# Kernel tuning notes

Hardware: AMD Instinct MI355X
Metric: run time of the kernel (lower is better)

Reference implementation:

```python
import jax, jax.numpy as jnp
import numpy as np

NG, NT, E = 2500, 20000, 640000
SRC_DIM, DST_DIM, HID, OUT, NCLS = 128, 500, 128, 128, 16


def setup_inputs() -> dict:
    key = jax.random.key(0)
    ks = jax.random.split(key, 11)
    d = {
        "gene_feats": jax.random.normal(ks[0], (NG, SRC_DIM), jnp.float32),
        "train_feats": jax.random.normal(ks[1], (NT, DST_DIM), jnp.float32),
        "edge_src": jax.random.randint(ks[2], (E,), 0, NG),
        "edge_dst": jax.random.randint(ks[3], (E,), 0, NT),
        # conv1: SAGEConv((src_dim, dst_dim) -> hidden)
        "W1_neigh": jax.random.normal(ks[4], (SRC_DIM, HID), jnp.float32) / np.sqrt(SRC_DIM),
        "W1_self": jax.random.normal(ks[5], (DST_DIM, HID), jnp.float32) / np.sqrt(DST_DIM),
        "b1": jnp.zeros((HID,), jnp.float32),
        # conv2: SAGEConv(hidden -> out); src input is the raw gene features
        "W2_neigh": jax.random.normal(ks[6], (HID, OUT), jnp.float32) / np.sqrt(HID),
        "W2_self": jax.random.normal(ks[7], (HID, OUT), jnp.float32) / np.sqrt(HID),
        "b2": jnp.zeros((OUT,), jnp.float32),
        # classifier MLP
        "Wc1": jax.random.normal(ks[8], (OUT, OUT), jnp.float32) / np.sqrt(OUT),
        "bc1": jnp.zeros((OUT,), jnp.float32),
        "Wc2": jax.random.normal(ks[9], (OUT, NCLS), jnp.float32) / np.sqrt(OUT),
        "bc2": jnp.zeros((NCLS,), jnp.float32),
    }
    return d


def _segment_mean(msgs, dst, num_segments):
    # mean over in-edges; isolated dst nodes get 0 (DGL convention)
    sums = jax.ops.segment_sum(msgs, dst, num_segments=num_segments)
    cnt = jax.ops.segment_sum(jnp.ones((msgs.shape[0],), msgs.dtype), dst,
                              num_segments=num_segments)
    return sums / jnp.maximum(cnt, 1.0)[:, None]


def reference(gene_feats, train_feats, edge_src, edge_dst,
              W1_neigh, W1_self, b1, W2_neigh, W2_self, b2,
              Wc1, bc1, Wc2, bc2):
    # mean-aggregate gene (src) features onto train (dst) nodes
    agg = _segment_mean(gene_feats[edge_src], edge_dst, NT)  # [NT, SRC_DIM]
    # conv1: fc_self(h_dst) + fc_neigh(mean_neigh) + bias, then ReLU
    h1 = jax.nn.relu(train_feats @ W1_self + agg @ W1_neigh + b1)  # [NT, HID]
    # conv2 reuses raw gene features as src -> same mean aggregation
    h2 = jax.nn.relu(h1 @ W2_self + agg @ W2_neigh + b2)  # [NT, OUT]
    # classifier: Linear -> ReLU -> Linear
    return jax.nn.relu(h2 @ Wc1 + bc1) @ Wc2 + bc2  # [NT, NCLS]
```

## Files before the change

### kernel.cpp

```cpp
#include <hip/hip_runtime.h>


#define NG 2500
#define NT 20000
#define NE 640000
#define NCLS 16
#define CAP 96
#define BCAP 1536
#define NBIN 625

typedef unsigned short u16;
typedef unsigned int u32;

typedef float f32x4 __attribute__((ext_vector_type(4)));
typedef __bf16 bf16x8 __attribute__((ext_vector_type(8)));

__device__ __forceinline__ float b2f(u16 u) { return __uint_as_float(((u32)u) << 16); }
__device__ __forceinline__ float blo(u32 p) { return __uint_as_float(p << 16); }
__device__ __forceinline__ float bhi(u32 p) { return __uint_as_float(p & 0xffff0000u); }
__device__ __forceinline__ u16 f2b(float f) {
    u32 u = __float_as_uint(f);
    return (u16)((u + 0x7fffu + ((u >> 16) & 1u)) >> 16);
}

#define B1N 81920
#define B2N 32768
#define B3N 16384
#define B4N 2048
#define NEB 625
#define GNB 625
#define PKB 520

__global__ __launch_bounds__(256) void k_prep(
    const int* __restrict__ edst,
    u32* __restrict__ hist,
    const float* __restrict__ gene, u32* __restrict__ GH32,
    const float* __restrict__ W1n, const float* __restrict__ W1s,
    const float* __restrict__ W2n, const float* __restrict__ W2s,
    const float* __restrict__ Wc1, const float* __restrict__ Wc2,
    u16* __restrict__ B1h, u16* __restrict__ B1l,
    u16* __restrict__ B2h, u16* __restrict__ B2l,
    u16* __restrict__ B3h, u16* __restrict__ B3l,
    u16* __restrict__ B4h, u16* __restrict__ B4l) {
    int blk = blockIdx.x, t = threadIdx.x;
    if (blk < NEB) {
        __shared__ u32 lh[NBIN];
        for (int i = t; i < NBIN; i += 256) lh[i] = 0;
        __syncthreads();
        int e0 = (blk * 256 + t) * 4;
        const int4 d4 = *(const int4*)(edst + e0);
        int dd[4] = {d4.x, d4.y, d4.z, d4.w};
#pragma unroll
        for (int i = 0; i < 4; ++i) {
            unsigned d = (unsigned)dd[i];
            if (d < NT) atomicAdd(&lh[d >> 5], 1u);
        }
        __syncthreads();
        for (int i = t; i < NBIN; i += 256)
            hist[(size_t)blk * NBIN + i] = lh[i];
        return;
    }
    if (blk < NEB + GNB) {
        int idx = (blk - NEB) * 256 + t;
        float2 v = ((const float2*)gene)[idx];
        GH32[idx] = (u32)f2b(v.x) | ((u32)f2b(v.y) << 16);
        return;
    }
    int idx = (blk - NEB - GNB) * 256 + t;
    float v = 0.f;
    u16 *ph = 0, *pl = 0;
    int off = 0;
    if (idx < B1N) {
        int j = idx & 7, l = (idx >> 3) & 63, rest = idx >> 9;
        int g = rest & 7, kk = rest >> 3;
        int k = kk * 32 + ((l >> 4) << 3) + j, n = (g << 4) + (l & 15);
        if (k < 500) v = W1s[k * 128 + n];
        else if (k >= 512) v = W1n[(k - 512) * 128 + n];
        ph = B1h; pl = B1l; off = idx;
    } else if (idx < B1N + B2N) {
        int e = idx - B1N;
        int j = e & 7, l = (e >> 3) & 63, rest = e >> 9;
        int g = rest & 7, kk = rest >> 3;
        int k = kk * 32 + ((l >> 4) << 3) + j, n = (g << 4) + (l & 15);
        v = (k < 128) ? W2s[k * 128 + n] : W2n[(k - 128) * 128 + n];
        ph = B2h; pl = B2l; off = e;
    } else if (idx < B1N + B2N + B3N) {
        int e = idx - (B1N + B2N);
        int j = e & 7, l = (e >> 3) & 63, rest = e >> 9;
        int g = rest & 7, kk = rest >> 3;
        int k = kk * 32 + ((l >> 4) << 3) + j, n = (g << 4) + (l & 15);
        v = Wc1[k * 128 + n];
        ph = B3h; pl = B3l; off = e;
    } else if (idx < B1N + B2N + B3N + B4N) {
        int e = idx - (B1N + B2N + B3N);
        int j = e & 7, l = (e >> 3) & 63, kk = e >> 9;
        int k = kk * 32 + ((l >> 4) << 3) + j, n = l & 15;
        v = Wc2[k * 16 + n];
        ph = B4h; pl = B4l; off = e;
    }
    if (ph) {
        u16 hi = f2b(v);
        u16 lo = f2b(v - b2f(hi));
        ph[off] = hi;
        pl[off] = lo;
    }
}

__global__ __launch_bounds__(256) void k_scan(
    const u32* __restrict__ hist, u32* __restrict__ boff,
    int* __restrict__ bcnt) {
    int bin = blockIdx.x, t = threadIdx.x;
    __shared__ u32 part[256];
    u32 s0 = 0, s1 = 0, s2 = 0;
    int i0 = 3 * t;
    if (i0 < NBIN) s0 = hist[(size_t)i0 * NBIN + bin];
    if (i0 + 1 < NBIN) s1 = hist[(size_t)(i0 + 1) * NBIN + bin];
    if (i0 + 2 < NBIN) s2 = hist[(size_t)(i0 + 2) * NBIN + bin];
    u32 mine = s0 + s1 + s2;
    part[t] = mine;
    __syncthreads();
    for (int off = 1; off < 256; off <<= 1) {
        u32 x = (t >= off) ? part[t - off] : 0u;
        __syncthreads();
        part[t] += x;
        __syncthreads();
    }
    u32 base = part[t] - mine;
    if (i0 < NBIN) boff[(size_t)bin * NBIN + i0] = base;
    if (i0 + 1 < NBIN) boff[(size_t)bin * NBIN + i0 + 1] = base + s0;
    if (i0 + 2 < NBIN) boff[(size_t)bin * NBIN + i0 + 2] = base + s0 + s1;
    if (t == 255) bcnt[bin] = (int)part[255];
}

__global__ __launch_bounds__(256) void k_scat(
    const int* __restrict__ esrc, const int* __restrict__ edst,
    const u32* __restrict__ boff, u32* __restrict__ bkt) {
    int blk = blockIdx.x, t = threadIdx.x;
    __shared__ u32 lcur[NBIN];
    for (int i = t; i < NBIN; i += 256) lcur[i] = 0;
    __syncthreads();
    int e0 = (blk * 256 + t) * 4;
    const int4 s4 = *(const int4*)(esrc + e0);
    const int4 d4 = *(const int4*)(edst + e0);
    int ss[4] = {s4.x, s4.y, s4.z, s4.w};
    int dd[4] = {d4.x, d4.y, d4.z, d4.w};
#pragma unroll
    for (int i = 0; i < 4; ++i) {
        unsigned d = (unsigned)dd[i];
        if (d < NT) {
            int bin = (int)(d >> 5);
            u32 rank = atomicAdd(&lcur[bin], 1u);
            u32 pos = boff[(size_t)bin * NBIN + blk] + rank;
            if (pos < BCAP)
                bkt[(size_t)bin * BCAP + pos] = ((d & 31u) << 16) | (u32)ss[i];
        }
    }
}

__global__ __launch_bounds__(512, 3) void k_mega(
    const int* __restrict__ bcnt, const u32* __restrict__ bkt,
    const u16* __restrict__ GH, const float* __restrict__ train,
    const u16* __restrict__ B1h, const u16* __restrict__ B1l,
    const u16* __restrict__ B2h, const u16* __restrict__ B2l,
    const u16* __restrict__ B3h, const u16* __restrict__ B3l,
    const u16* __restrict__ B4h, const u16* __restrict__ B4l,
    const float* __restrict__ b1, const float* __restrict__ b2,
    const float* __restrict__ bc1, const float* __restrict__ bc2,
    float* __restrict__ out) {
    __shared__ __align__(16) u16 SMEM[26112];
    __shared__ __align__(16) u16 SRT[32 * CAP];
    __shared__ int POS[32];
    u16* SAGh = SMEM;
    u16* SAGl = SMEM + 4352;
    u16* S1h = SMEM + 8704;
    u16* S1l = SMEM + 13056;
    u16* S2h = SMEM + 17408;
    u16* S2l = SMEM + 21760;
    u16* TS = SMEM + 8704;

    int t = threadIdx.x;
    int row0 = blockIdx.x * 32;

    float4 st[8];
    {
        const float4* tb = (const float4*)(train + (size_t)row0 * 500);
#pragma unroll
        for (int i = 0; i < 7; ++i) st[i] = tb[t + i * 512];
        if (t < 416) st[7] = tb[t + 3584];
    }

    if (t < 32) POS[t] = 0;
    int bc = bcnt[blockIdx.x];
    if (bc > BCAP) bc = BCAP;
    __syncthreads();

    for (int i = t; i < bc; i += 512) {
        u32 e = bkt[(size_t)blockIdx.x * BCAP + i];
        int r = (int)(e >> 16);
        int p = atomicAdd(&POS[r], 1);
        if (p < CAP) SRT[r * CAP + p] = (u16)(e & 0xffffu);
    }

    {
        u32* T32 = (u32*)TS;
#pragma unroll
        for (int i = 0; i < 8; ++i) {
            int idx = t + i * 512;
            if (i == 7 && t >= 416) break;
            int r = idx / 125, c4 = idx - r * 125;
            int base = r * 260 + c4 * 2;
            T32[base] = (u32)f2b(st[i].x) | ((u32)f2b(st[i].y) << 16);
            T32[base + 1] = (u32)f2b(st[i].z) | ((u32)f2b(st[i].w) << 16);
        }
        if (t < 192) {
            int r = t / 6, c4 = t - r * 6;
            T32[r * 260 + 250 + c4] = 0;
        }
    }
    __syncthreads();

    int lane = t & 63, g = t >> 6;
    int m = lane & 15, q = lane >> 4, n16 = lane & 15;
    int gr = t >> 4, cg = t & 15;

    int ctrue = POS[gr];
    int c = ctrue > CAP ? CAP : ctrue;
    const u16* crow = SRT + gr * CAP;
    int nfull = c >> 3;
    uint4 i40 = *(const uint4*)(crow);
    uint4 i41 = *(const uint4*)(crow + 8);
    uint4 i42 = *(const uint4*)(crow + 16);
    uint4 i43 = *(const uint4*)(crow + 24);
    float a[8];
#pragma unroll
    for (int p = 0; p < 8; ++p) a[p] = 0.f;

    int hr0 = m * 136 + q * 8;
    int hr1 = (16 + m) * 136 + q * 8;
    int cr0 = q * 4, cr1 = 16 + q * 4;
    const f32x4 z4 = {0.f, 0.f, 0.f, 0.f};
    f32x4 acc0 = z4, acc1 = z4;
    const u16* tA0 = TS + m * 520 + q * 8;
    const u16* tA1 = TS + (16 + m) * 520 + q * 8;

#define ACC(p)                                      \
    do {                                            \
        a[0] += blo((p).x); a[1] += bhi((p).x);     \
        a[2] += blo((p).y); a[3] += bhi((p).y);     \
        a[4] += blo((p).z); a[5] += bhi((p).z);     \
        a[6] += blo((p).w); a[7] += bhi((p).w);     \
    } while (0)

    auto GHLoad = [&](int s) -> uint4 {
        return *(const uint4*)(GH + (size_t)s * 128 + cg * 8);
    };
    uint4 P0, P1, P2, P3, P4, P5, P6, P7;
    auto issue8 = [&](uint4 iq) {
        P0 = GHLoad((int)(iq.x & 0xffffu)); P1 = GHLoad((int)(iq.x >> 16));
        P2 = GHLoad((int)(iq.y & 0xffffu)); P3 = GHLoad((int)(iq.y >> 16));
        P4 = GHLoad((int)(iq.z & 0xffffu)); P5 = GHLoad((int)(iq.z >> 16));
        P6 = GHLoad((int)(iq.w & 0xffffu)); P7 = GHLoad((int)(iq.w >> 16));
    };
    auto acc8 = [&]() {
        ACC(P0); ACC(P1); ACC(P2); ACC(P3);
        ACC(P4); ACC(P5); ACC(P6); ACC(P7);
    };
    auto kk4 = [&](int base) {
#pragma unroll
        for (int kk = base; kk < base + 4; ++kk) {
            bf16x8 a0 = *(const bf16x8*)(tA0 + kk * 32);
            bf16x8 a1 = *(const bf16x8*)(tA1 + kk * 32);
            size_t bo = ((size_t)(kk * 8 + g) * 64 + lane) * 8;
            bf16x8 bh = *(const bf16x8*)(B1h + bo);
            bf16x8 bl = *(const bf16x8*)(B1l + bo);
            acc0 = __builtin_amdgcn_mfma_f32_16x16x32_bf16(a0, bh, acc0, 0, 0, 0);
            acc0 = __builtin_amdgcn_mfma_f32_16x16x32_bf16(a0, bl, acc0, 0, 0, 0);
            acc1 = __builtin_amdgcn_mfma_f32_16x16x32_bf16(a1, bh, acc1, 0, 0, 0);
            acc1 = __builtin_amdgcn_mfma_f32_16x16x32_bf16(a1, bl, acc1, 0, 0, 0);
        }
    };

    if (nfull > 0) issue8(i40);
    kk4(0);
    if (nfull > 0) acc8();
    if (nfull > 1) issue8(i41);
    kk4(4);
    if (nfull > 1) acc8();
    if (nfull > 2) issue8(i42);
    kk4(8);
    if (nfull > 2) acc8();
    if (nfull > 3) issue8(i43);
    kk4(12);
    if (nfull > 3) acc8();
    for (int b = 4; b < nfull; ++b) {
        uint4 i4 = *(const uint4*)(crow + b * 8);
        issue8(i4);
        acc8();
    }
    {
        int j = nfull * 8;
        if (j < c) {
            uint4 i4 = *(const uint4*)(crow + j);
            u32 w[4] = {i4.x, i4.y, i4.z, i4.w};
#pragma unroll
            for (int k = 0; k < 8; ++k) {
                int s = (int)((w[k >> 1] >> ((k & 1) * 16)) & 0xffffu);
                bool live = (j + k) < c;
                s = live ? s : 0;
                uint4 p = GHLoad(s);
                if (live) ACC(p);
            }
        }
    }
#undef ACC

    {
        float inv = (ctrue > 0) ? 1.f / (float)ctrue : 0.f;
        int base = (gr * 136 + cg * 8) >> 1;
        u32* SH = (u32*)SAGh;
        u32* SL = (u32*)SAGl;
#pragma unroll
        for (int p = 0; p < 4; ++p) {
            float x = a[2 * p] * inv, y = a[2 * p + 1] * inv;
            u16 hx = f2b(x), hy = f2b(y);
            SH[base + p] = (u32)hx | ((u32)hy << 16);
            SL[base + p] = (u32)f2b(x - b2f(hx)) | ((u32)f2b(y - b2f(hy)) << 16);
        }
    }
    __syncthreads();

#pragma unroll
    for (int kk = 16; kk < 20; ++kk) {
        int o = (kk - 16) * 32;
        bf16x8 ah0 = *(const bf16x8*)(SAGh + hr0 + o);
        bf16x8 al0 = *(const bf16x8*)(SAGl + hr0 + o);
        bf16x8 ah1 = *(const bf16x8*)(SAGh + hr1 + o);
        bf16x8 al1 = *(const bf16x8*)(SAGl + hr1 + o);
        size_t bo = ((size_t)(kk * 8 + g) * 64 + lane) * 8;
        bf16x8 bh = *(const bf16x8*)(B1h + bo);
        bf16x8 bl = *(const bf16x8*)(B1l + bo);
        acc0 = __builtin_amdgcn_mfma_f32_16x16x32_bf16(ah0, bh, acc0, 0, 0, 0);
        acc0 = __builtin_amdgcn_mfma_f32_16x16x32_bf16(ah0, bl, acc0, 0, 0, 0);
        acc0 = __builtin_amdgcn_mfma_f32_16x16x32_bf16(al0, bh, acc0, 0, 0, 0);
        acc1 = __builtin_amdgcn_mfma_f32_16x16x32_bf16(ah1, bh, acc1, 0, 0, 0);
        acc1 = __builtin_amdgcn_mfma_f32_16x16x32_bf16(ah1, bl, acc1, 0, 0, 0);
        acc1 = __builtin_amdgcn_mfma_f32_16x16x32_bf16(al1, bh, acc1, 0, 0, 0);
    }
    {
        int n = g * 16 + n16;
        float bias = b1[n];
#pragma unroll
        for (int rg = 0; rg < 4; ++rg) {
            float v0 = acc0[rg] + bias; v0 = v0 > 0.f ? v0 : 0.f;
            float v1 = acc1[rg] + bias; v1 = v1 > 0.f ? v1 : 0.f;
            u16 h0 = f2b(v0), h1v = f2b(v1);
            S1h[(cr0 + rg) * 136 + n] = h0; S1l[(cr0 + rg) * 136 + n] = f2b(v0 - b2f(h0));
            S1h[(cr1 + rg) * 136 + n] = h1v; S1l[(cr1 + rg) * 136 + n] = f2b(v1 - b2f(h1v));
        }
    }
    __syncthreads();

    acc0 = z4; acc1 = z4;
#pragma unroll
    for (int kk = 0; kk < 8; ++kk) {
        const u16* Ph = (kk < 4) ? S1h : SAGh;
        const u16* Pl = (kk < 4) ? S1l : SAGl;
        int o = (kk & 3) * 32;
        bf16x8 ah0 = *(const bf16x8*)(Ph + hr0 + o);
        bf16x8 al0 = *(const bf16x8*)(Pl + hr0 + o);
        bf16x8 ah1 = *(const bf16x8*)(Ph + hr1 + o);
        bf16x8 al1 = *(const bf16x8*)(Pl + hr1 + o);
        size_t bo = ((size_t)(kk * 8 + g) * 64 + lane) * 8;
        bf16x8 bh = *(const bf16x8*)(B2h + bo);
        bf16x8 bl = *(const bf16x8*)(B2l + bo);
        acc0 = __builtin_amdgcn_mfma_f32_16x16x32_bf16(ah0, bh, acc0, 0, 0, 0);
        acc0 = __builtin_amdgcn_mfma_f32_16x16x32_bf16(ah0, bl, acc0, 0, 0, 0);
        acc0 = __builtin_amdgcn_mfma_f32_16x16x32_bf16(al0, bh, acc0, 0, 0, 0);
        acc1 = __builtin_amdgcn_mfma_f32_16x16x32_bf16(ah1, bh, acc1, 0, 0, 0);
        acc1 = __builtin_amdgcn_mfma_f32_16x16x32_bf16(ah1, bl, acc1, 0, 0, 0);
        acc1 = __builtin_amdgcn_mfma_f32_16x16x32_bf16(al1, bh, acc1, 0, 0, 0);
    }
    {
        int n = g * 16 + n16;
        float bias = b2[n];
#pragma unroll
        for (int rg = 0; rg < 4; ++rg) {
            float v0 = acc0[rg] + bias; v0 = v0 > 0.f ? v0 : 0.f;
            float v1 = acc1[rg] + bias; v1 = v1 > 0.f ? v1 : 0.f;
            u16 h0 = f2b(v0), h1v = f2b(v1);
            S2h[(cr0 + rg) * 136 + n] = h0; S2l[(cr0 + rg) * 136 + n] = f2b(v0 - b2f(h0));
            S2h[(cr1 + rg) * 136 + n] = h1v; S2l[(cr1 + rg) * 136 + n] = f2b(v1 - b2f(h1v));
        }
    }
    __syncthreads();

    acc0 = z4; acc1 = z4;
#pragma unroll
    for (int kk = 0; kk < 4; ++kk) {
        int o = kk * 32;
        bf16x8 ah0 = *(const bf16x8*)(S2h + hr0 + o);
        bf16x8 al0 = *(const bf16x8*)(S2l + hr0 + o);
        bf16x8 ah1 = *(const bf16x8*)(S2h + hr1 + o);
        bf16x8 al1 = *(const bf16x8*)(S2l + hr1 + o);
        size_t bo = ((size_t)(kk * 8 + g) * 64 + lane) * 8;
        bf16x8 bh = *(const bf16x8*)(B3h + bo);
        bf16x8 bl = *(const bf16x8*)(B3l + bo);
        acc0 = __builtin_amdgcn_mfma_f32_16x16x32_bf16(ah0, bh, acc0, 0, 0, 0);
        acc0 = __builtin_amdgcn_mfma_f32_16x16x32_bf16(ah0, bl, acc0, 0, 0, 0);
        acc0 = __builtin_amdgcn_mfma_f32_16x16x32_bf16(al0, bh, acc0, 0, 0, 0);
        acc1 = __builtin_amdgcn_mfma_f32_16x16x32_bf16(ah1, bh, acc1, 0, 0, 0);
        acc1 = __builtin_amdgcn_mfma_f32_16x16x32_bf16(ah1, bl, acc1, 0, 0, 0);
        acc1 = __builtin_amdgcn_mfma_f32_16x16x32_bf16(al1, bh, acc1, 0, 0, 0);
    }
    {
        int n = g * 16 + n16;
        float bias = bc1[n];
#pragma unroll
        for (int rg = 0; rg < 4; ++rg) {
            float v0 = acc0[rg] + bias; v0 = v0 > 0.f ? v0 : 0.f;
            float v1 = acc1[rg] + bias; v1 = v1 > 0.f ? v1 : 0.f;
            u16 h0 = f2b(v0), h1v = f2b(v1);
            S1h[(cr0 + rg) * 136 + n] = h0; S1l[(cr0 + rg) * 136 + n] = f2b(v0 - b2f(h0));
            S1h[(cr1 + rg) * 136 + n] = h1v; S1l[(cr1 + rg) * 136 + n] = f2b(v1 - b2f(h1v));
        }
    }
    __syncthreads();

    if (g < 2) {
        int hr = (g == 0) ? hr0 : hr1;
        int cr = (g == 0) ? cr0 : cr1;
        f32x4 a4 = z4;
#pragma unroll
        for (int kk = 0; kk < 4; ++kk) {
            bf16x8 ah = *(const bf16x8*)(S1h + hr + kk * 32);
            bf16x8 al = *(const bf16x8*)(S1l + hr + kk * 32);
            size_t bo = ((size_t)kk * 64 + lane) * 8;
            bf16x8 bh = *(const bf16x8*)(B4h + bo);
            bf16x8 bl = *(const bf16x8*)(B4l + bo);
            a4 = __builtin_amdgcn_mfma_f32_16x16x32_bf16(ah, bh, a4, 0, 0, 0);
            a4 = __builtin_amdgcn_mfma_f32_16x16x32_bf16(ah, bl, a4, 0, 0, 0);
            a4 = __builtin_amdgcn_mfma_f32_16x16x32_bf16(al, bh, a4, 0, 0, 0);
        }
        float bias = bc2[n16];
#pragma unroll
        for (int rg = 0; rg < 4; ++rg)
            out[(size_t)(row0 + cr + rg) * NCLS + n16] = a4[rg] + bias;
    }
}

extern "C" void kernel_launch(void* const* d_in, const int* in_sizes, int n_in,
                              void* d_out, int out_size, void* d_ws, size_t ws_size,
                              hipStream_t stream) {
    const float* gene = (const float*)d_in[0];
    const float* train = (const float*)d_in[1];
    const int* esrc = (const int*)d_in[2];
    const int* edst = (const int*)d_in[3];

    char* ws = (char*)d_ws;
    int* bcnt = (int*)(ws + 0);
    u32* hist = (u32*)(ws + 4096);
    u32* boff = (u32*)(ws + 1566720);
    u32* bkt = (u32*)(ws + 3129344);
    u16* GH = (u16*)(ws + 6969344);
    u16* B1h = (u16*)(ws + 7609344);
    u16* B1l = (u16*)(ws + 7773184);
    u16* B2h = (u16*)(ws + 7937024);
    u16* B2l = (u16*)(ws + 8002560);
    u16* B3h = (u16*)(ws + 8068096);
    u16* B3l = (u16*)(ws + 8100864);
    u16* B4h = (u16*)(ws + 8133632);
    u16* B4l = (u16*)(ws + 8137728);

    k_prep<<<NEB + GNB + PKB, 256, 0, stream>>>(
        edst, hist, gene, (u32*)GH,
        (const float*)d_in[4], (const float*)d_in[5], (const float*)d_in[7],
        (const float*)d_in[8], (const float*)d_in[10], (const float*)d_in[12],
        B1h, B1l, B2h, B2l, B3h, B3l, B4h, B4l);
    k_scan<<<NBIN, 256, 0, stream>>>(hist, boff, bcnt);
    k_scat<<<NEB, 256, 0, stream>>>(esrc, edst, boff, bkt);
    k_mega<<<NT / 32, 512, 0, stream>>>(
        bcnt, bkt, GH, train, B1h, B1l, B2h, B2l, B3h, B3l, B4h, B4l,
        (const float*)d_in[6], (const float*)d_in[9], (const float*)d_in[11],
        (const float*)d_in[13], (float*)d_out);
}
```

Baseline: 155.1 us.

## Split fused mega kernel into separate aggregation and MLP kernels

Splits the single fused kernel into two. k_agg gathers the neighbour features with 16 rows per 256-thread block and writes the mean aggregate, as bf16 hi/lo pairs, to a global workspace. k_mlp then reads the aggregate and runs the MFMA layers. The aim is to raise occupancy and parallelism for the latency-bound gather, which was interleaved with the MFMA work in the fused kernel. In exchange it adds a kernel launch and a global round trip of the aggregate (about 10 MB written and read back), and each bucket is now scanned twice, once per half-block.

```diff
diff --git a/kernel.cpp b/kernel.cpp
--- a/kernel.cpp
+++ b/kernel.cpp
@@ -157,72 +157,32 @@
     }
 }
 
-__global__ __launch_bounds__(512, 3) void k_mega(
+__global__ __launch_bounds__(256, 8) void k_agg(
     const int* __restrict__ bcnt, const u32* __restrict__ bkt,
-    const u16* __restrict__ GH, const float* __restrict__ train,
-    const u16* __restrict__ B1h, const u16* __restrict__ B1l,
-    const u16* __restrict__ B2h, const u16* __restrict__ B2l,
-    const u16* __restrict__ B3h, const u16* __restrict__ B3l,
-    const u16* __restrict__ B4h, const u16* __restrict__ B4l,
-    const float* __restrict__ b1, const float* __restrict__ b2,
-    const float* __restrict__ bc1, const float* __restrict__ bc2,
-    float* __restrict__ out) {
-    __shared__ __align__(16) u16 SMEM[26112];
-    __shared__ __align__(16) u16 SRT[32 * CAP];
-    __shared__ int POS[32];
-    u16* SAGh = SMEM;
-    u16* SAGl = SMEM + 4352;
-    u16* S1h = SMEM + 8704;
-    u16* S1l = SMEM + 13056;
-    u16* S2h = SMEM + 17408;
-    u16* S2l = SMEM + 21760;
-    u16* TS = SMEM + 8704;
-
+    const u16* __restrict__ GH,
+    u32* __restrict__ AGH, u32* __restrict__ AGL) {
+    __shared__ __align__(16) u16 SRT[16 * CAP];
+    __shared__ int POS[16];
     int t = threadIdx.x;
-    int row0 = blockIdx.x * 32;
-
-    float4 st[8];
-    {
-        const float4* tb = (const float4*)(train + (size_t)row0 * 500);
-#pragma unroll
-        for (int i = 0; i < 7; ++i) st[i] = tb[t + i * 512];
-        if (t < 416) st[7] = tb[t + 3584];
-    }
-
-    if (t < 32) POS[t] = 0;
-    int bc = bcnt[blockIdx.x];
+    int bk = blockIdx.x >> 1, half = blockIdx.x & 1;
+
+    if (t < 16) POS[t] = 0;
+    int bc = bcnt[bk];
     if (bc > BCAP) bc = BCAP;
     __syncthreads();
 
-    for (int i = t; i < bc; i += 512) {
-        u32 e = bkt[(size_t)blockIdx.x * BCAP + i];
-        int r = (int)(e >> 16);
-        int p = atomicAdd(&POS[r], 1);
-        if (p < CAP) SRT[r * CAP + p] = (u16)(e & 0xffffu);
-    }
-
-    {
-        u32* T32 = (u32*)TS;
-#pragma unroll
-        for (int i = 0; i < 8; ++i) {
-            int idx = t + i * 512;
-            if (i == 7 && t >= 416) break;
-            int r = idx / 125, c4 = idx - r * 125;
-            int base = r * 260 + c4 * 2;
-            T32[base] = (u32)f2b(st[i].x) | ((u32)f2b(st[i].y) << 16);
-            T32[base + 1] = (u32)f2b(st[i].z) | ((u32)f2b(st[i].w) << 16);
-        }
-        if (t < 192) {
-            int r = t / 6, c4 = t - r * 6;
-            T32[r * 260 + 250 + c4] = 0;
-        }
-    }
-    __syncthreads();
-
-    int lane = t & 63, g = t >> 6;
-    int m = lane & 15, q = lane >> 4, n16 = lane & 15;
+    int rlo = half * 16;
+    for (int i = t; i < bc; i += 256) {
+        u32 e = bkt[(size_t)bk * BCAP + i];
+        int r = (int)(e >> 16) - rlo;
+        if ((unsigned)r < 16u) {
+            int p = atomicAdd(&POS[r], 1);
+            if (p < CAP) SRT[r * CAP + p] = (u16)(e & 0xffffu);
+        }
+    }
+    __syncthreads();
+
     int gr = t >> 4, cg = t & 15;
-
     int ctrue = POS[gr];
     int c = ctrue > CAP ? CAP : ctrue;
     const u16* crow = SRT + gr * CAP;
@@ -235,6 +195,125 @@
 #pragma unroll
     for (int p = 0; p < 8; ++p) a[p] = 0.f;
 
+#define ACC(p)                                      \
+    do {                                            \
+        a[0] += blo((p).x); a[1] += bhi((p).x);     \
+        a[2] += blo((p).y); a[3] += bhi((p).y);     \
+        a[4] += blo((p).z); a[5] += bhi((p).z);     \
+        a[6] += blo((p).w); a[7] += bhi((p).w);     \
+    } while (0)
+    auto GHLoad = [&](int s) -> uint4 {
+        return *(const uint4*)(GH + (size_t)s * 128 + cg * 8);
+    };
+    auto batch8 = [&](uint4 iq) {
+        uint4 P0 = GHLoad((int)(iq.x & 0xffffu));
+        uint4 P1 = GHLoad((int)(iq.x >> 16));
+        uint4 P2 = GHLoad((int)(iq.y & 0xffffu));
+        uint4 P3 = GHLoad((int)(iq.y >> 16));
+        uint4 P4 = GHLoad((int)(iq.z & 0xffffu));
+        uint4 P5 = GHLoad((int)(iq.z >> 16));
+        uint4 P6 = GHLoad((int)(iq.w & 0xffffu));
+        uint4 P7 = GHLoad((int)(iq.w >> 16));
+        ACC(P0); ACC(P1); ACC(P2); ACC(P3);
+        ACC(P4); ACC(P5); ACC(P6); ACC(P7);
+    };
+
+    if (nfull > 0) batch8(i40);
+    if (nfull > 1) batch8(i41);
+    if (nfull > 2) batch8(i42);
+    if (nfull > 3) batch8(i43);
+    for (int b = 4; b < nfull; ++b) batch8(*(const uint4*)(crow + b * 8));
+    {
+        int j = nfull * 8;
+        if (j < c) {
+            uint4 i4 = *(const uint4*)(crow + j);
+            u32 w[4] = {i4.x, i4.y, i4.z, i4.w};
+#pragma unroll
+            for (int k = 0; k < 8; ++k) {
+                int s = (int)((w[k >> 1] >> ((k & 1) * 16)) & 0xffffu);
+                bool live = (j + k) < c;
+                s = live ? s : 0;
+                uint4 p = GHLoad(s);
+                if (live) ACC(p);
+            }
+        }
+    }
+#undef ACC
+
+    float inv = (ctrue > 0) ? 1.f / (float)ctrue : 0.f;
+    size_t base = (size_t)(blockIdx.x * 16 + gr) * 64 + cg * 4;
+#pragma unroll
+    for (int p = 0; p < 4; ++p) {
+        float x = a[2 * p] * inv, y = a[2 * p + 1] * inv;
+        u16 hx = f2b(x), hy = f2b(y);
+        AGH[base + p] = (u32)hx | ((u32)hy << 16);
+        AGL[base + p] = (u32)f2b(x - b2f(hx)) | ((u32)f2b(y - b2f(hy)) << 16);
+    }
+}
+
+__global__ __launch_bounds__(512, 4) void k_mlp(
+    const u32* __restrict__ AGH, const u32* __restrict__ AGL,
+    const float* __restrict__ train,
+    const u16* __restrict__ B1h, const u16* __restrict__ B1l,
+    const u16* __restrict__ B2h, const u16* __restrict__ B2l,
+    const u16* __restrict__ B3h, const u16* __restrict__ B3l,
+    const u16* __restrict__ B4h, const u16* __restrict__ B4l,
+    const float* __restrict__ b1, const float* __restrict__ b2,
+    const float* __restrict__ bc1, const float* __restrict__ bc2,
+    float* __restrict__ out) {
+    __shared__ __align__(16) u16 SMEM[26112];
+    u16* SAGh = SMEM;
+    u16* SAGl = SMEM + 4352;
+    u16* S1h = SMEM + 8704;
+    u16* S1l = SMEM + 13056;
+    u16* S2h = SMEM + 17408;
+    u16* S2l = SMEM + 21760;
+    u16* TS = SMEM + 8704;
+
+    int t = threadIdx.x;
+    int row0 = blockIdx.x * 32;
+
+    float4 st[8];
+    {
+        const float4* tb = (const float4*)(train + (size_t)row0 * 500);
+#pragma unroll
+        for (int i = 0; i < 7; ++i) st[i] = tb[t + i * 512];
+        if (t < 416) st[7] = tb[t + 3584];
+    }
+    uint4 ah4 = ((const uint4*)AGH)[(size_t)row0 * 16 + t];
+    uint4 al4 = ((const uint4*)AGL)[(size_t)row0 * 16 + t];
+
+    {
+        u32* T32 = (u32*)TS;
+#pragma unroll
+        for (int i = 0; i < 8; ++i) {
+            int idx = t + i * 512;
+            if (i == 7 && t >= 416) break;
+            int r = idx / 125, c4 = idx - r * 125;
+            int base = r * 260 + c4 * 2;
+            T32[base] = (u32)f2b(st[i].x) | ((u32)f2b(st[i].y) << 16);
+            T32[base + 1] = (u32)f2b(st[i].z) | ((u32)f2b(st[i].w) << 16);
+        }
+        if (t < 192) {
+            int r = t / 6, c4 = t - r * 6;
+            T32[r * 260 + 250 + c4] = 0;
+        }
+    }
+    {
+        int r = t >> 4, c16 = t & 15;
+        int base = r * 68 + c16 * 4;
+        u32* SH = (u32*)SAGh;
+        u32* SL = (u32*)SAGl;
+        SH[base] = ah4.x; SH[base + 1] = ah4.y;
+        SH[base + 2] = ah4.z; SH[base + 3] = ah4.w;
+        SL[base] = al4.x; SL[base + 1] = al4.y;
+        SL[base + 2] = al4.z; SL[base + 3] = al4.w;
+    }
+    __syncthreads();
+
+    int lane = t & 63, g = t >> 6;
+    int m = lane & 15, q = lane >> 4, n16 = lane & 15;
+
     int hr0 = m * 136 + q * 8;
     int hr1 = (16 + m) * 136 + q * 8;
     int cr0 = q * 4, cr1 = 16 + q * 4;
@@ -243,92 +322,18 @@
     const u16* tA0 = TS + m * 520 + q * 8;
     const u16* tA1 = TS + (16 + m) * 520 + q * 8;
 
-#define ACC(p)                                      \
-    do {                                            \
-        a[0] += blo((p).x); a[1] += bhi((p).x);     \
-        a[2] += blo((p).y); a[3] += bhi((p).y);     \
-        a[4] += blo((p).z); a[5] += bhi((p).z);     \
-        a[6] += blo((p).w); a[7] += bhi((p).w);     \
-    } while (0)
-
-    auto GHLoad = [&](int s) -> uint4 {
-        return *(const uint4*)(GH + (size_t)s * 128 + cg * 8);
-    };
-    uint4 P0, P1, P2, P3, P4, P5, P6, P7;
-    auto issue8 = [&](uint4 iq) {
-        P0 = GHLoad((int)(iq.x & 0xffffu)); P1 = GHLoad((int)(iq.x >> 16));
-        P2 = GHLoad((int)(iq.y & 0xffffu)); P3 = GHLoad((int)(iq.y >> 16));
-        P4 = GHLoad((int)(iq.z & 0xffffu)); P5 = GHLoad((int)(iq.z >> 16));
-        P6 = GHLoad((int)(iq.w & 0xffffu)); P7 = GHLoad((int)(iq.w >> 16));
-    };
-    auto acc8 = [&]() {
-        ACC(P0); ACC(P1); ACC(P2); ACC(P3);
-        ACC(P4); ACC(P5); ACC(P6); ACC(P7);
-    };
-    auto kk4 = [&](int base) {
-#pragma unroll
-        for (int kk = base; kk < base + 4; ++kk) {
-            bf16x8 a0 = *(const bf16x8*)(tA0 + kk * 32);
-            bf16x8 a1 = *(const bf16x8*)(tA1 + kk * 32);
-            size_t bo = ((size_t)(kk * 8 + g) * 64 + lane) * 8;
-            bf16x8 bh = *(const bf16x8*)(B1h + bo);
-            bf16x8 bl = *(const bf16x8*)(B1l + bo);
-            acc0 = __builtin_amdgcn_mfma_f32_16x16x32_bf16(a0, bh, acc0, 0, 0, 0);
-            acc0 = __builtin_amdgcn_mfma_f32_16x16x32_bf16(a0, bl, acc0, 0, 0, 0);
-            acc1 = __builtin_amdgcn_mfma_f32_16x16x32_bf16(a1, bh, acc1, 0, 0, 0);
-            acc1 = __builtin_amdgcn_mfma_f32_16x16x32_bf16(a1, bl, acc1, 0, 0, 0);
-        }
-    };
-
-    if (nfull > 0) issue8(i40);
-    kk4(0);
-    if (nfull > 0) acc8();
-    if (nfull > 1) issue8(i41);
-    kk4(4);
-    if (nfull > 1) acc8();
-    if (nfull > 2) issue8(i42);
-    kk4(8);
-    if (nfull > 2) acc8();
-    if (nfull > 3) issue8(i43);
-    kk4(12);
-    if (nfull > 3) acc8();
-    for (int b = 4; b < nfull; ++b) {
-        uint4 i4 = *(const uint4*)(crow + b * 8);
-        issue8(i4);
-        acc8();
-    }
-    {
-        int j = nfull * 8;
-        if (j < c) {
-            uint4 i4 = *(const uint4*)(crow + j);
-            u32 w[4] = {i4.x, i4.y, i4.z, i4.w};
-#pragma unroll
-            for (int k = 0; k < 8; ++k) {
-                int s = (int)((w[k >> 1] >> ((k & 1) * 16)) & 0xffffu);
-                bool live = (j + k) < c;
-                s = live ? s : 0;
-                uint4 p = GHLoad(s);
-                if (live) ACC(p);
-            }
-        }
-    }
-#undef ACC
-
-    {
-        float inv = (ctrue > 0) ? 1.f / (float)ctrue : 0.f;
-        int base = (gr * 136 + cg * 8) >> 1;
-        u32* SH = (u32*)SAGh;
-        u32* SL = (u32*)SAGl;
-#pragma unroll
-        for (int p = 0; p < 4; ++p) {
-            float x = a[2 * p] * inv, y = a[2 * p + 1] * inv;
-            u16 hx = f2b(x), hy = f2b(y);
-            SH[base + p] = (u32)hx | ((u32)hy << 16);
-            SL[base + p] = (u32)f2b(x - b2f(hx)) | ((u32)f2b(y - b2f(hy)) << 16);
-        }
-    }
-    __syncthreads();
-
+#pragma unroll
+    for (int kk = 0; kk < 16; ++kk) {
+        bf16x8 a0 = *(const bf16x8*)(tA0 + kk * 32);
+        bf16x8 a1 = *(const bf16x8*)(tA1 + kk * 32);
+        size_t bo = ((size_t)(kk * 8 + g) * 64 + lane) * 8;
+        bf16x8 bh = *(const bf16x8*)(B1h + bo);
+        bf16x8 bl = *(const bf16x8*)(B1l + bo);
+        acc0 = __builtin_amdgcn_mfma_f32_16x16x32_bf16(a0, bh, acc0, 0, 0, 0);
+        acc0 = __builtin_amdgcn_mfma_f32_16x16x32_bf16(a0, bl, acc0, 0, 0, 0);
+        acc1 = __builtin_amdgcn_mfma_f32_16x16x32_bf16(a1, bh, acc1, 0, 0, 0);
+        acc1 = __builtin_amdgcn_mfma_f32_16x16x32_bf16(a1, bl, acc1, 0, 0, 0);
+    }
 #pragma unroll
     for (int kk = 16; kk < 20; ++kk) {
         int o = (kk - 16) * 32;
@@ -346,6 +351,7 @@
         acc1 = __builtin_amdgcn_mfma_f32_16x16x32_bf16(ah1, bl, acc1, 0, 0, 0);
         acc1 = __builtin_amdgcn_mfma_f32_16x16x32_bf16(al1, bh, acc1, 0, 0, 0);
     }
+    __syncthreads();
     {
         int n = g * 16 + n16;
         float bias = b1[n];
@@ -462,14 +468,16 @@
     u32* boff = (u32*)(ws + 1566720);
     u32* bkt = (u32*)(ws + 3129344);
     u16* GH = (u16*)(ws + 6969344);
-    u16* B1h = (u16*)(ws + 7609344);
-    u16* B1l = (u16*)(ws + 7773184);
-    u16* B2h = (u16*)(ws + 7937024);
-    u16* B2l = (u16*)(ws + 8002560);
-    u16* B3h = (u16*)(ws + 8068096);
-    u16* B3l = (u16*)(ws + 8100864);
-    u16* B4h = (u16*)(ws + 8133632);
-    u16* B4l = (u16*)(ws + 8137728);
+    u32* AGH = (u32*)(ws + 7609344);
+    u32* AGL = (u32*)(ws + 12729344);
+    u16* B1h = (u16*)(ws + 17849344);
+    u16* B1l = (u16*)(ws + 18013184);
+    u16* B2h = (u16*)(ws + 18177024);
+    u16* B2l = (u16*)(ws + 18242560);
+    u16* B3h = (u16*)(ws + 18308096);
+    u16* B3l = (u16*)(ws + 18340864);
+    u16* B4h = (u16*)(ws + 18373632);
+    u16* B4l = (u16*)(ws + 18377728);
 
     k_prep<<<NEB + GNB + PKB, 256, 0, stream>>>(
         edst, hist, gene, (u32*)GH,
@@ -478,8 +486,9 @@
         B1h, B1l, B2h, B2l, B3h, B3l, B4h, B4l);
     k_scan<<<NBIN, 256, 0, stream>>>(hist, boff, bcnt);
     k_scat<<<NEB, 256, 0, stream>>>(esrc, edst, boff, bkt);
-    k_mega<<<NT / 32, 512, 0, stream>>>(
-        bcnt, bkt, GH, train, B1h, B1l, B2h, B2l, B3h, B3l, B4h, B4l,
+    k_agg<<<NT / 16, 256, 0, stream>>>(bcnt, bkt, GH, AGH, AGL);
+    k_mlp<<<NT / 32, 512, 0, stream>>>(
+        AGH, AGL, train, B1h, B1l, B2h, B2l, B3h, B3l, B4h, B4l,
         (const float*)d_in[6], (const float*)d_in[9], (const float*)d_in[11],
         (const float*)d_in[13], (float*)d_out);
 }
```

After: 153.8 us, median of 2. Within noise of the previous version (-0.8%).
